# Kernel optimization log

Measured on AMD Instinct MI355X. Metric: run time of the kernel, lower is better.

## Reference

```python
import jax, jax.numpy as jnp
import numpy as np


def setup_inputs() -> dict:
    key = jax.random.key(0)
    ks = jax.random.split(key, 4)
    B, H, W, C = 4, 64, 64, 256
    d = C // 8
    x = jax.random.normal(ks[0], (B, H, W, C), dtype=jnp.float32)
    wq = jax.random.normal(ks[1], (C, d), dtype=jnp.float32) * (1.0 / np.sqrt(C))
    wk = jax.random.normal(ks[2], (C, d), dtype=jnp.float32) * (1.0 / np.sqrt(C))
    wv = jax.random.normal(ks[3], (C, C), dtype=jnp.float32) * (1.0 / np.sqrt(C))
    bq = jnp.zeros((d,), dtype=jnp.float32)
    bk = jnp.zeros((d,), dtype=jnp.float32)
    bv = jnp.zeros((C,), dtype=jnp.float32)
    return {"x": x, "wq": wq, "bq": bq, "wk": wk, "bk": bk, "wv": wv, "bv": bv}


def reference(x, wq, bq, wk, bk, wv, bv):
    # x: [B, H, W, C] (channels-last, as in Keras Conv2D default)
    B, H, W, C = x.shape
    N = H * W
    xf = x.reshape(B, N, C)                      # 1x1 conv == per-pixel matmul
    q = xf @ wq + bq                             # [B, N, C//8]
    k = xf @ wk + bk                             # [B, N, C//8]
    v = xf @ wv + bv                             # [B, N, C]
    # NOTE: original module applies NO 1/sqrt(d) scaling.
    attn = jax.nn.softmax(jnp.einsum('bnd,bmd->bnm', q, k), axis=-1)  # [B, N, N]
    out = jnp.einsum('bnm,bmc->bnc', attn, v)    # [B, N, C]
    return out.reshape(B, H, W, C) + x
```

## Files before the change

kernel.cpp:

```cpp
#include <hip/hip_runtime.h>
#include <stdint.h>

typedef _Float16 f16;
typedef f16 half8 __attribute__((ext_vector_type(8)));
typedef f16 half4 __attribute__((ext_vector_type(4)));
typedef float floatx4 __attribute__((ext_vector_type(4)));

#define MFMA_F16(A, B, Cc) __builtin_amdgcn_mfma_f32_16x16x32_f16((A), (B), (Cc), 0, 0, 0)

static constexpr int NB  = 4;
static constexpr int NN  = 4096;
static constexpr int NC  = 256;
static constexpr int ND  = 32;
static constexpr int PIX = NB * NN;
static constexpr int NS  = 4;
static constexpr int KS  = NN / NS;

__device__ f16 g_WbT[320 * 256];
__device__ f16 g_Qh[(size_t)PIX * ND];
__device__ f16 g_Kh[(size_t)PIX * ND];
__device__ f16 g_VbT[(size_t)NB * NC * NN];
__device__ f16 g_Of[(size_t)NS * PIX * NC];
__device__ float g_m[NS * PIX];
__device__ float g_l[NS * PIX];

__device__ inline void gl2lds16(const f16* g, f16* l) {
  __builtin_amdgcn_global_load_lds(
      (const __attribute__((address_space(1))) void*)g,
      (__attribute__((address_space(3))) void*)l, 16, 0, 0);
}

__global__ __launch_bounds__(256) void prep_weights(const float* __restrict__ wq,
                                                    const float* __restrict__ wk,
                                                    const float* __restrict__ wv) {
  const int tid = blockIdx.x * 256 + threadIdx.x;
  if (tid >= 320 * 256) return;
  const int j = tid >> 8;
  const int k = tid & 255;
  float v;
  if (j < 32)      v = wq[k * 32 + j];
  else if (j < 64) v = wk[k * 32 + (j - 32)];
  else             v = wv[k * 256 + (j - 64)];
  g_WbT[j * 256 + k] = (f16)v;
}

__global__ __launch_bounds__(256) void proj_qkv(const float* __restrict__ x,
                                                const float* __restrict__ bq,
                                                const float* __restrict__ bk,
                                                const float* __restrict__ bv) {
  __shared__ f16 xs[64 * 32];
  __shared__ f16 wsT[160 * 32];
  __shared__ f16 vt[160 * 64];

  const int tid  = threadIdx.x;
  const int lane = tid & 63;
  const int wid  = tid >> 6;
  const int qd   = lane >> 4;
  const int c16  = lane & 15;
  const int p0   = blockIdx.x * 64;
  const int half = blockIdx.y;
  const int j0   = half * 160;
  const floatx4 zero4 = {0.f, 0.f, 0.f, 0.f};

  floatx4 acc[10];
#pragma unroll
  for (int i = 0; i < 10; ++i) acc[i] = zero4;

  for (int kk = 0; kk < 256; kk += 32) {
    {
      const int r = tid >> 2, g = tid & 3;
      const floatx4* s4 = (const floatx4*)(x + (size_t)(p0 + r) * NC + kk + g * 8);
      const floatx4 xa = s4[0], xb = s4[1];
      half8 h;
      h[0] = (f16)xa[0]; h[1] = (f16)xa[1]; h[2] = (f16)xa[2]; h[3] = (f16)xa[3];
      h[4] = (f16)xb[0]; h[5] = (f16)xb[1]; h[6] = (f16)xb[2]; h[7] = (f16)xb[3];
      *(half8*)&xs[r * 32 + g * 8] = h;
    }
#pragma unroll
    for (int i = 0; i < 5; ++i) {
      const int cid = tid + 256 * i;
      const int j = cid >> 3, m = cid & 7;
      *(half4*)&wsT[j * 32 + m * 4] = *(const half4*)&g_WbT[(j0 + j) * 256 + kk + m * 4];
    }
    __syncthreads();
    const half8 a = *(const half8*)&xs[(wid * 16 + c16) * 32 + qd * 8];
#pragma unroll
    for (int nt = 0; nt < 10; ++nt) {
      const half8 bfr = *(const half8*)&wsT[(nt * 16 + c16) * 32 + qd * 8];
      acc[nt] = MFMA_F16(a, bfr, acc[nt]);
    }
    __syncthreads();
  }

#pragma unroll
  for (int nt = 0; nt < 10; ++nt) {
    const int j = j0 + nt * 16 + c16;
    const float bias = (j < 32) ? bq[j] : (j < 64) ? bk[j - 32] : bv[j - 64];
#pragma unroll
    for (int r = 0; r < 4; ++r) {
      const int rl = wid * 16 + qd * 4 + r;
      const int p  = p0 + rl;
      const float val = acc[nt][r] + bias;
      if (j < 32) {
        g_Qh[(size_t)p * ND + j] = (f16)(val * 1.44269504f);
      } else if (j < 64) {
        g_Kh[(size_t)p * ND + (j - 32)] = (f16)val;
      } else {
        vt[(j - 64 - half * 96) * 64 + rl] = (f16)val;
      }
    }
  }
  __syncthreads();
  const int b    = p0 >> 12;
  const int n0   = p0 & (NN - 1);
  const int ncol = half ? 160 : 96;
  const int c0   = half ? 96 : 0;
  const int nit  = (ncol * 16) >> 8;
  for (int i = 0; i < nit; ++i) {
    const int cid = tid + 256 * i;
    const int c = cid >> 4, m = cid & 15;
    *(half4*)(g_VbT + ((size_t)(b * NC + c0 + c)) * NN + n0 + m * 4) =
        *(const half4*)&vt[c * 64 + m * 4];
  }
}

__global__ __launch_bounds__(256, 2) void attn_split(void) {
  __shared__ f16 vsT[256 * 64];
  __shared__ f16 ps[4][2][16 * 64];

  const int tid  = threadIdx.x;
  const int lane = tid & 63;
  const int wid  = tid >> 6;
  const int qd   = lane >> 4;
  const int c16  = lane & 15;
  const int b    = blockIdx.y;
  const int s    = blockIdx.z;
  const int q0   = blockIdx.x * 128 + wid * 32;
  const int sx7  = c16 & 7;
  const floatx4 zero4 = {0.f, 0.f, 0.f, 0.f};

  const int vrow = wid * 64 + (lane >> 3);
  const int vchk = (lane & 7) ^ ((lane >> 3) & 7);
  const f16* vlane = g_VbT + ((size_t)(b * NC + vrow)) * NN + vchk * 8;
  f16* vdst = &vsT[(size_t)wid * 4096 + (size_t)0];

  half8 qf[2];
#pragma unroll
  for (int g = 0; g < 2; ++g)
    qf[g] = *(const half8*)(g_Qh + ((size_t)(b * NN + q0 + g * 16 + c16)) * ND + qd * 8);

  floatx4 acc[2][16];
#pragma unroll
  for (int g = 0; g < 2; ++g)
#pragma unroll
    for (int i = 0; i < 16; ++i) acc[g][i] = zero4;
  float m_i[2] = {-1e30f, -1e30f};
  float l_p[2] = {0.f, 0.f};

  const int kbeg = s * KS, kend = (s + 1) * KS;

#pragma unroll
  for (int i = 0; i < 8; ++i)
    gl2lds16(vlane + kbeg + i * 8 * NN, vdst + i * 512);
  half8 kreg[4];
#pragma unroll
  for (int a = 0; a < 4; ++a)
    kreg[a] = *(const half8*)(g_Kh + ((size_t)(b * NN + kbeg + a * 16 + c16)) * ND + qd * 8);

  for (int k0 = kbeg; k0 < kend; k0 += 64) {
    floatx4 st[2][4];
#pragma unroll
    for (int g = 0; g < 2; ++g)
#pragma unroll
      for (int a = 0; a < 4; ++a) st[g][a] = MFMA_F16(kreg[a], qf[g], zero4);

    float tm[2];
#pragma unroll
    for (int g = 0; g < 2; ++g) {
      float t0 = fmaxf(fmaxf(st[g][0][0], st[g][0][1]), fmaxf(st[g][0][2], st[g][0][3]));
      float t1 = fmaxf(fmaxf(st[g][1][0], st[g][1][1]), fmaxf(st[g][1][2], st[g][1][3]));
      float t2 = fmaxf(fmaxf(st[g][2][0], st[g][2][1]), fmaxf(st[g][2][2], st[g][2][3]));
      float t3 = fmaxf(fmaxf(st[g][3][0], st[g][3][1]), fmaxf(st[g][3][2], st[g][3][3]));
      tm[g] = fmaxf(fmaxf(t0, t1), fmaxf(t2, t3));
    }
    if (__any(tm[0] > m_i[0] || tm[1] > m_i[1])) {
#pragma unroll
      for (int g = 0; g < 2; ++g) {
        float tr = tm[g];
        tr = fmaxf(tr, __shfl_xor(tr, 16));
        tr = fmaxf(tr, __shfl_xor(tr, 32));
        const float m_new = (tr > m_i[g]) ? tr + 5.0f : m_i[g];
        const float alpha = exp2f(m_i[g] - m_new);
        m_i[g] = m_new;
        l_p[g] *= alpha;
        float a4[4];
#pragma unroll
        for (int r = 0; r < 4; ++r) a4[r] = __shfl(alpha, qd * 4 + r);
#pragma unroll
        for (int ct = 0; ct < 16; ++ct)
#pragma unroll
          for (int r = 0; r < 4; ++r) acc[g][ct][r] *= a4[r];
      }
    }

#pragma unroll
    for (int g = 0; g < 2; ++g) {
      float ts = 0.f;
#pragma unroll
      for (int a = 0; a < 4; ++a) {
        half4 h;
#pragma unroll
        for (int r = 0; r < 4; ++r) {
          const float p = exp2f(st[g][a][r] - m_i[g]);
          ts += p;
          h[r] = (f16)p;
        }
        const int pc = ((a * 2 + (qd >> 1)) ^ sx7) * 8 + (qd & 1) * 4;
        *(half4*)&ps[wid][g][c16 * 64 + pc] = h;
      }
      l_p[g] += ts;
    }

    __syncthreads();

    const int k0n = (k0 + 64 < kend) ? (k0 + 64) : kbeg;
    half8 knew[4];
#pragma unroll
    for (int a = 0; a < 4; ++a)
      knew[a] = *(const half8*)(g_Kh + ((size_t)(b * NN + k0n + a * 16 + c16)) * ND + qd * 8);

    half8 pa[2][2];
#pragma unroll
    for (int g = 0; g < 2; ++g)
#pragma unroll
      for (int kh = 0; kh < 2; ++kh)
        pa[g][kh] = *(const half8*)&ps[wid][g][c16 * 64 + ((kh * 4 + qd) ^ sx7) * 8];
#pragma unroll
    for (int ct = 0; ct < 16; ++ct) {
#pragma unroll
      for (int kh = 0; kh < 2; ++kh) {
        const half8 bfr =
            *(const half8*)&vsT[(ct * 16 + c16) * 64 + ((kh * 4 + qd) ^ sx7) * 8];
        acc[0][ct] = MFMA_F16(pa[0][kh], bfr, acc[0][ct]);
        acc[1][ct] = MFMA_F16(pa[1][kh], bfr, acc[1][ct]);
      }
    }
    __syncthreads();

    if (k0 + 64 < kend) {
#pragma unroll
      for (int i = 0; i < 8; ++i)
        gl2lds16(vlane + (k0 + 64) + i * 8 * NN, vdst + i * 512);
    }
#pragma unroll
    for (int a = 0; a < 4; ++a) kreg[a] = knew[a];
  }

#pragma unroll
  for (int g = 0; g < 2; ++g) {
    float l = l_p[g];
    l += __shfl_xor(l, 16);
    l += __shfl_xor(l, 32);
    if (qd == 0) {
      const int row = b * NN + q0 + g * 16 + c16;
      g_m[s * PIX + row] = m_i[g];
      g_l[s * PIX + row] = l;
    }
    float linv[4];
#pragma unroll
    for (int r = 0; r < 4; ++r) linv[r] = 1.0f / __shfl(l, qd * 4 + r);
#pragma unroll
    for (int ct = 0; ct < 16; ++ct)
#pragma unroll
      for (int r = 0; r < 4; ++r) {
        const int qrow = q0 + g * 16 + qd * 4 + r;
        const int c = ct * 16 + c16;
        g_Of[((size_t)(s * PIX + b * NN + qrow)) * NC + c] = (f16)(acc[g][ct][r] * linv[r]);
      }
  }
}

__global__ __launch_bounds__(256) void combine(const float* __restrict__ x,
                                               float* __restrict__ out) {
  const int tid  = threadIdx.x;
  const int lane = tid & 63;
  const int wid  = tid >> 6;
  const int row  = blockIdx.x * 8 + wid * 2 + (lane >> 5);
  const int c    = (lane & 31) * 8;

  float m[NS], l[NS], M = -1e30f;
#pragma unroll
  for (int s = 0; s < NS; ++s) {
    m[s] = g_m[s * PIX + row];
    l[s] = g_l[s * PIX + row];
    M = fmaxf(M, m[s]);
  }
  float w[NS], den = 0.f;
#pragma unroll
  for (int s = 0; s < NS; ++s) { w[s] = l[s] * exp2f(m[s] - M); den += w[s]; }
  const float inv = 1.0f / den;

  float a[8];
#pragma unroll
  for (int j = 0; j < 8; ++j) a[j] = 0.f;
#pragma unroll
  for (int s = 0; s < NS; ++s) {
    const half8 h = *(const half8*)&g_Of[((size_t)(s * PIX + row)) * NC + c];
    const float ws = w[s] * inv;
#pragma unroll
    for (int j = 0; j < 8; ++j) a[j] += ws * (float)h[j];
  }
  const floatx4 x0 = *(const floatx4*)&x[(size_t)row * NC + c];
  const floatx4 x1 = *(const floatx4*)&x[(size_t)row * NC + c + 4];
  floatx4 o0, o1;
#pragma unroll
  for (int j = 0; j < 4; ++j) { o0[j] = a[j] + x0[j]; o1[j] = a[j + 4] + x1[j]; }
  *(floatx4*)&out[(size_t)row * NC + c] = o0;
  *(floatx4*)&out[(size_t)row * NC + c + 4] = o1;
}

extern "C" void kernel_launch(void* const* d_in, const int* in_sizes, int n_in,
                              void* d_out, int out_size, void* d_ws, size_t ws_size,
                              hipStream_t stream) {
  (void)in_sizes; (void)n_in; (void)d_ws; (void)ws_size; (void)out_size;
  const float* x  = (const float*)d_in[0];
  const float* wq = (const float*)d_in[1];
  const float* bq = (const float*)d_in[2];
  const float* wk = (const float*)d_in[3];
  const float* bk = (const float*)d_in[4];
  const float* wv = (const float*)d_in[5];
  const float* bv = (const float*)d_in[6];
  float* out = (float*)d_out;

  hipLaunchKernelGGL(prep_weights, dim3(320), dim3(256), 0, stream, wq, wk, wv);
  hipLaunchKernelGGL(proj_qkv, dim3(256, 2), dim3(256), 0, stream, x, bq, bk, bv);
  hipLaunchKernelGGL(attn_split, dim3(NN / 128, NB, NS), dim3(256), 0, stream);
  hipLaunchKernelGGL(combine, dim3(PIX / 8), dim3(256), 0, stream, x, out);
}
```

Measured before the change: 163.0 us.

## Load projection operands directly from global and vectorize Q/K/V stores via LDS

The projection kernel stops staging x and weight tiles through shared memory. Each lane now loads its MFMA A fragment straight from x and its B fragments straight from the fp16 weight buffer, which removes two barriers per k-step. Q and K outputs are staged in LDS and written with 16-byte row stores instead of scattered 2-byte stores. The V transpose write-out is widened from half4 to half8. Without LDS sharing, each wave re-reads the weights from global/L2, which raises cache traffic.

```diff
diff --git a/kernel.cpp b/kernel.cpp
--- a/kernel.cpp
+++ b/kernel.cpp
@@ -48,9 +48,9 @@
                                                 const float* __restrict__ bq,
                                                 const float* __restrict__ bk,
                                                 const float* __restrict__ bv) {
-  __shared__ f16 xs[64 * 32];
-  __shared__ f16 wsT[160 * 32];
   __shared__ f16 vt[160 * 64];
+  __shared__ f16 qt[64 * 32];
+  __shared__ f16 kt[64 * 32];
 
   const int tid  = threadIdx.x;
   const int lane = tid & 63;
@@ -66,30 +66,21 @@
 #pragma unroll
   for (int i = 0; i < 10; ++i) acc[i] = zero4;
 
+  const float* xrow = x + (size_t)(p0 + wid * 16 + c16) * NC;
+
+#pragma unroll
   for (int kk = 0; kk < 256; kk += 32) {
-    {
-      const int r = tid >> 2, g = tid & 3;
-      const floatx4* s4 = (const floatx4*)(x + (size_t)(p0 + r) * NC + kk + g * 8);
-      const floatx4 xa = s4[0], xb = s4[1];
-      half8 h;
-      h[0] = (f16)xa[0]; h[1] = (f16)xa[1]; h[2] = (f16)xa[2]; h[3] = (f16)xa[3];
-      h[4] = (f16)xb[0]; h[5] = (f16)xb[1]; h[6] = (f16)xb[2]; h[7] = (f16)xb[3];
-      *(half8*)&xs[r * 32 + g * 8] = h;
-    }
-#pragma unroll
-    for (int i = 0; i < 5; ++i) {
-      const int cid = tid + 256 * i;
-      const int j = cid >> 3, m = cid & 7;
-      *(half4*)&wsT[j * 32 + m * 4] = *(const half4*)&g_WbT[(j0 + j) * 256 + kk + m * 4];
-    }
-    __syncthreads();
-    const half8 a = *(const half8*)&xs[(wid * 16 + c16) * 32 + qd * 8];
+    const floatx4* s4 = (const floatx4*)(xrow + kk + qd * 8);
+    const floatx4 xa = s4[0], xb = s4[1];
+    half8 a;
+    a[0] = (f16)xa[0]; a[1] = (f16)xa[1]; a[2] = (f16)xa[2]; a[3] = (f16)xa[3];
+    a[4] = (f16)xb[0]; a[5] = (f16)xb[1]; a[6] = (f16)xb[2]; a[7] = (f16)xb[3];
 #pragma unroll
     for (int nt = 0; nt < 10; ++nt) {
-      const half8 bfr = *(const half8*)&wsT[(nt * 16 + c16) * 32 + qd * 8];
+      const half8 bfr =
+          *(const half8*)&g_WbT[(size_t)(j0 + nt * 16 + c16) * 256 + kk + qd * 8];
       acc[nt] = MFMA_F16(a, bfr, acc[nt]);
     }
-    __syncthreads();
   }
 
 #pragma unroll
@@ -99,28 +90,36 @@
 #pragma unroll
     for (int r = 0; r < 4; ++r) {
       const int rl = wid * 16 + qd * 4 + r;
-      const int p  = p0 + rl;
       const float val = acc[nt][r] + bias;
       if (j < 32) {
-        g_Qh[(size_t)p * ND + j] = (f16)(val * 1.44269504f);
+        qt[rl * 32 + j] = (f16)(val * 1.44269504f);
       } else if (j < 64) {
-        g_Kh[(size_t)p * ND + (j - 32)] = (f16)val;
+        kt[rl * 32 + (j - 32)] = (f16)val;
       } else {
         vt[(j - 64 - half * 96) * 64 + rl] = (f16)val;
       }
     }
   }
   __syncthreads();
+
+  if (half == 0) {
+    const int row = tid >> 2, ch = tid & 3;
+    *(half8*)(g_Qh + (size_t)(p0 + row) * ND + ch * 8) =
+        *(const half8*)&qt[row * 32 + ch * 8];
+    *(half8*)(g_Kh + (size_t)(p0 + row) * ND + ch * 8) =
+        *(const half8*)&kt[row * 32 + ch * 8];
+  }
+
   const int b    = p0 >> 12;
   const int n0   = p0 & (NN - 1);
   const int ncol = half ? 160 : 96;
   const int c0   = half ? 96 : 0;
-  const int nit  = (ncol * 16) >> 8;
+  const int nit  = ncol >> 5;
   for (int i = 0; i < nit; ++i) {
     const int cid = tid + 256 * i;
-    const int c = cid >> 4, m = cid & 15;
-    *(half4*)(g_VbT + ((size_t)(b * NC + c0 + c)) * NN + n0 + m * 4) =
-        *(const half4*)&vt[c * 64 + m * 4];
+    const int c = cid >> 3, m = cid & 7;
+    *(half8*)(g_VbT + ((size_t)(b * NC + c0 + c)) * NN + n0 + m * 8) =
+        *(const half8*)&vt[c * 64 + m * 8];
   }
 }
 
```

Measured after the change: 181.6 us. +11.4%, slower.

## Fuse split-K combine into attention kernel via last-block atomic counter

Applied to the files above, without the earlier changes.

The separate combine kernel is removed. Each attention block now fences its partial results and increments a per-tile atomic counter, and the last of the NS split blocks for a query tile merges the partial outputs with x and writes the final result. This removes one kernel launch and lets the merge overlap with other attention blocks still running. In exchange the merge runs serialized on one block per tile, the block adds fence and atomic overhead, and correctness depends on the counter being reset after each call.

```diff
diff --git a/kernel.cpp b/kernel.cpp
--- a/kernel.cpp
+++ b/kernel.cpp
@@ -23,6 +23,7 @@
 __device__ f16 g_Of[(size_t)NS * PIX * NC];
 __device__ float g_m[NS * PIX];
 __device__ float g_l[NS * PIX];
+__device__ int   g_cnt[NB * (NN / 128)];
 
 __device__ inline void gl2lds16(const f16* g, f16* l) {
   __builtin_amdgcn_global_load_lds(
@@ -124,7 +125,8 @@
   }
 }
 
-__global__ __launch_bounds__(256, 2) void attn_split(void) {
+__global__ __launch_bounds__(256, 2) void attn_split(const float* __restrict__ x,
+                                                     float* __restrict__ out) {
   __shared__ f16 vsT[256 * 64];
   __shared__ f16 ps[4][2][16 * 64];
 
@@ -278,45 +280,65 @@
         g_Of[((size_t)(s * PIX + b * NN + qrow)) * NC + c] = (f16)(acc[g][ct][r] * linv[r]);
       }
   }
-}
-
-__global__ __launch_bounds__(256) void combine(const float* __restrict__ x,
-                                               float* __restrict__ out) {
-  const int tid  = threadIdx.x;
-  const int lane = tid & 63;
-  const int wid  = tid >> 6;
-  const int row  = blockIdx.x * 8 + wid * 2 + (lane >> 5);
-  const int c    = (lane & 31) * 8;
-
-  float m[NS], l[NS], M = -1e30f;
-#pragma unroll
-  for (int s = 0; s < NS; ++s) {
-    m[s] = g_m[s * PIX + row];
-    l[s] = g_l[s * PIX + row];
-    M = fmaxf(M, m[s]);
-  }
-  float w[NS], den = 0.f;
-#pragma unroll
-  for (int s = 0; s < NS; ++s) { w[s] = l[s] * exp2f(m[s] - M); den += w[s]; }
-  const float inv = 1.0f / den;
-
-  float a[8];
-#pragma unroll
-  for (int j = 0; j < 8; ++j) a[j] = 0.f;
-#pragma unroll
-  for (int s = 0; s < NS; ++s) {
-    const half8 h = *(const half8*)&g_Of[((size_t)(s * PIX + row)) * NC + c];
-    const float ws = w[s] * inv;
-#pragma unroll
-    for (int j = 0; j < 8; ++j) a[j] += ws * (float)h[j];
-  }
-  const floatx4 x0 = *(const floatx4*)&x[(size_t)row * NC + c];
-  const floatx4 x1 = *(const floatx4*)&x[(size_t)row * NC + c + 4];
-  floatx4 o0, o1;
-#pragma unroll
-  for (int j = 0; j < 4; ++j) { o0[j] = a[j] + x0[j]; o1[j] = a[j + 4] + x1[j]; }
-  *(floatx4*)&out[(size_t)row * NC + c] = o0;
-  *(floatx4*)&out[(size_t)row * NC + c + 4] = o1;
+
+  __threadfence();
+  __syncthreads();
+  const int cidx = b * (NN / 128) + blockIdx.x;
+  float* wsm   = (float*)&ps[0][0][0];
+  int*   s_old = (int*)(wsm + 512);
+  if (tid == 0) {
+    *s_old = __hip_atomic_fetch_add(&g_cnt[cidx], 1, __ATOMIC_ACQ_REL,
+                                    __HIP_MEMORY_SCOPE_AGENT);
+  }
+  __syncthreads();
+  if (*s_old != NS - 1) return;
+
+  const int rbase = b * NN + blockIdx.x * 128;
+
+  if (tid < 128) {
+    const int row = rbase + tid;
+    float mm[NS], ll[NS], M = -1e30f;
+#pragma unroll
+    for (int sp = 0; sp < NS; ++sp) {
+      mm[sp] = g_m[sp * PIX + row];
+      ll[sp] = g_l[sp * PIX + row];
+      M = fmaxf(M, mm[sp]);
+    }
+    float w[NS], den = 0.f;
+#pragma unroll
+    for (int sp = 0; sp < NS; ++sp) { w[sp] = ll[sp] * exp2f(mm[sp] - M); den += w[sp]; }
+    const float inv = 1.0f / den;
+#pragma unroll
+    for (int sp = 0; sp < NS; ++sp) wsm[tid * 4 + sp] = w[sp] * inv;
+  }
+  __syncthreads();
+
+#pragma unroll
+  for (int i = 0; i < 16; ++i) {
+    const int gi  = tid + 256 * i;
+    const int rl  = gi >> 5;
+    const int cc  = (gi & 31) * 8;
+    const int row = rbase + rl;
+    float a[8];
+#pragma unroll
+    for (int j = 0; j < 8; ++j) a[j] = 0.f;
+#pragma unroll
+    for (int sp = 0; sp < NS; ++sp) {
+      const half8 h = *(const half8*)&g_Of[((size_t)(sp * PIX + row)) * NC + cc];
+      const float ws = wsm[rl * 4 + sp];
+#pragma unroll
+      for (int j = 0; j < 8; ++j) a[j] += ws * (float)h[j];
+    }
+    const floatx4 x0 = *(const floatx4*)&x[(size_t)row * NC + cc];
+    const floatx4 x1 = *(const floatx4*)&x[(size_t)row * NC + cc + 4];
+    floatx4 o0, o1;
+#pragma unroll
+    for (int j = 0; j < 4; ++j) { o0[j] = a[j] + x0[j]; o1[j] = a[j + 4] + x1[j]; }
+    *(floatx4*)&out[(size_t)row * NC + cc] = o0;
+    *(floatx4*)&out[(size_t)row * NC + cc + 4] = o1;
+  }
+
+  if (tid == 0) g_cnt[cidx] = 0;
 }
 
 extern "C" void kernel_launch(void* const* d_in, const int* in_sizes, int n_in,
@@ -334,6 +356,5 @@
 
   hipLaunchKernelGGL(prep_weights, dim3(320), dim3(256), 0, stream, wq, wk, wv);
   hipLaunchKernelGGL(proj_qkv, dim3(256, 2), dim3(256), 0, stream, x, bq, bk, bv);
-  hipLaunchKernelGGL(attn_split, dim3(NN / 128, NB, NS), dim3(256), 0, stream);
-  hipLaunchKernelGGL(combine, dim3(PIX / 8), dim3(256), 0, stream, x, out);
-}
+  hipLaunchKernelGGL(attn_split, dim3(NN / 128, NB, NS), dim3(256), 0, stream, x, out);
+}
```

Result: slower. 275.3 us (+68.9%).

## Double-buffer QKV projection with async LDS loads and split output columns four ways

Applied to the files above, without the earlier changes.

The projection kernel now splits the 320 output columns into four 80-wide slices instead of two 160-wide ones, doubling the grid and lowering per-block accumulator and LDS use so more blocks can be resident. It double-buffers the x and weight tiles: weights are copied straight into LDS with the global-to-LDS helper, and the next x chunk is loaded in registers while MFMAs run on the current chunk. One barrier per step replaces two. The V transpose write-out now uses 8-wide stores. In exchange, each x tile is read and converted twice as often across blocks.

```diff
diff --git a/kernel.cpp b/kernel.cpp
--- a/kernel.cpp
+++ b/kernel.cpp
@@ -44,13 +44,13 @@
   g_WbT[j * 256 + k] = (f16)v;
 }
 
-__global__ __launch_bounds__(256) void proj_qkv(const float* __restrict__ x,
-                                                const float* __restrict__ bq,
-                                                const float* __restrict__ bk,
-                                                const float* __restrict__ bv) {
-  __shared__ f16 xs[64 * 32];
-  __shared__ f16 wsT[160 * 32];
-  __shared__ f16 vt[160 * 64];
+__global__ __launch_bounds__(256, 4) void proj_qkv(const float* __restrict__ x,
+                                                   const float* __restrict__ bq,
+                                                   const float* __restrict__ bk,
+                                                   const float* __restrict__ bv) {
+  __shared__ f16 xs[2][64 * 32];
+  __shared__ f16 wsT[2][80 * 32];
+  __shared__ f16 vt[80 * 64];
 
   const int tid  = threadIdx.x;
   const int lane = tid & 63;
@@ -58,42 +58,62 @@
   const int qd   = lane >> 4;
   const int c16  = lane & 15;
   const int p0   = blockIdx.x * 64;
-  const int half = blockIdx.y;
-  const int j0   = half * 160;
+  const int q    = blockIdx.y;
+  const int j0   = q * 80;
   const floatx4 zero4 = {0.f, 0.f, 0.f, 0.f};
 
-  floatx4 acc[10];
-#pragma unroll
-  for (int i = 0; i < 10; ++i) acc[i] = zero4;
-
-  for (int kk = 0; kk < 256; kk += 32) {
-    {
-      const int r = tid >> 2, g = tid & 3;
-      const floatx4* s4 = (const floatx4*)(x + (size_t)(p0 + r) * NC + kk + g * 8);
-      const floatx4 xa = s4[0], xb = s4[1];
+  const int sr = tid >> 2, sg = tid & 3;
+  const float* xsrc = x + (size_t)(p0 + sr) * NC + sg * 8;
+  const f16* wsrc = g_WbT + (size_t)(j0 + (lane >> 2)) * 256 + (lane & 3) * 8;
+
+  floatx4 acc[5];
+#pragma unroll
+  for (int i = 0; i < 5; ++i) acc[i] = zero4;
+
+  {
+    const floatx4* s4 = (const floatx4*)xsrc;
+    const floatx4 xa = s4[0], xb = s4[1];
+#pragma unroll
+    for (int grp = wid; grp < 5; grp += 4)
+      gl2lds16(wsrc + (size_t)grp * 16 * 256, &wsT[0][grp * 512]);
+    half8 h;
+    h[0] = (f16)xa[0]; h[1] = (f16)xa[1]; h[2] = (f16)xa[2]; h[3] = (f16)xa[3];
+    h[4] = (f16)xb[0]; h[5] = (f16)xb[1]; h[6] = (f16)xb[2]; h[7] = (f16)xb[3];
+    *(half8*)&xs[0][sr * 32 + sg * 8] = h;
+  }
+
+  for (int c = 0; c < 8; ++c) {
+    const int cur = c & 1;
+    __syncthreads();
+
+    floatx4 xa, xb;
+    const bool pf = (c < 7);
+    if (pf) {
+      const floatx4* s4 = (const floatx4*)(xsrc + (c + 1) * 32);
+      xa = s4[0]; xb = s4[1];
+#pragma unroll
+      for (int grp = wid; grp < 5; grp += 4)
+        gl2lds16(wsrc + (size_t)grp * 16 * 256 + (c + 1) * 32,
+                 &wsT[cur ^ 1][grp * 512]);
+    }
+
+    const half8 a = *(const half8*)&xs[cur][(wid * 16 + c16) * 32 + qd * 8];
+#pragma unroll
+    for (int nt = 0; nt < 5; ++nt) {
+      const half8 bfr = *(const half8*)&wsT[cur][(nt * 16 + c16) * 32 + qd * 8];
+      acc[nt] = MFMA_F16(a, bfr, acc[nt]);
+    }
+
+    if (pf) {
       half8 h;
       h[0] = (f16)xa[0]; h[1] = (f16)xa[1]; h[2] = (f16)xa[2]; h[3] = (f16)xa[3];
       h[4] = (f16)xb[0]; h[5] = (f16)xb[1]; h[6] = (f16)xb[2]; h[7] = (f16)xb[3];
-      *(half8*)&xs[r * 32 + g * 8] = h;
-    }
-#pragma unroll
-    for (int i = 0; i < 5; ++i) {
-      const int cid = tid + 256 * i;
-      const int j = cid >> 3, m = cid & 7;
-      *(half4*)&wsT[j * 32 + m * 4] = *(const half4*)&g_WbT[(j0 + j) * 256 + kk + m * 4];
-    }
-    __syncthreads();
-    const half8 a = *(const half8*)&xs[(wid * 16 + c16) * 32 + qd * 8];
-#pragma unroll
-    for (int nt = 0; nt < 10; ++nt) {
-      const half8 bfr = *(const half8*)&wsT[(nt * 16 + c16) * 32 + qd * 8];
-      acc[nt] = MFMA_F16(a, bfr, acc[nt]);
-    }
-    __syncthreads();
-  }
-
-#pragma unroll
-  for (int nt = 0; nt < 10; ++nt) {
+      *(half8*)&xs[cur ^ 1][sr * 32 + sg * 8] = h;
+    }
+  }
+
+#pragma unroll
+  for (int nt = 0; nt < 5; ++nt) {
     const int j = j0 + nt * 16 + c16;
     const float bias = (j < 32) ? bq[j] : (j < 64) ? bk[j - 32] : bv[j - 64];
 #pragma unroll
@@ -106,21 +126,21 @@
       } else if (j < 64) {
         g_Kh[(size_t)p * ND + (j - 32)] = (f16)val;
       } else {
-        vt[(j - 64 - half * 96) * 64 + rl] = (f16)val;
+        const int vloc = (q == 0) ? (nt * 16 + c16 - 64) : (nt * 16 + c16);
+        vt[vloc * 64 + rl] = (f16)val;
       }
     }
   }
   __syncthreads();
+
   const int b    = p0 >> 12;
   const int n0   = p0 & (NN - 1);
-  const int ncol = half ? 160 : 96;
-  const int c0   = half ? 96 : 0;
-  const int nit  = (ncol * 16) >> 8;
-  for (int i = 0; i < nit; ++i) {
-    const int cid = tid + 256 * i;
-    const int c = cid >> 4, m = cid & 15;
-    *(half4*)(g_VbT + ((size_t)(b * NC + c0 + c)) * NN + n0 + m * 4) =
-        *(const half4*)&vt[c * 64 + m * 4];
+  const int vt0  = q ? (80 * q - 64) : 0;
+  const int ncol = q ? 80 : 16;
+  for (int i = tid; i < ncol * 8; i += 256) {
+    const int cc = i >> 3, m = i & 7;
+    *(half8*)(g_VbT + ((size_t)(b * NC + vt0 + cc)) * NN + n0 + m * 8) =
+        *(const half8*)&vt[cc * 64 + m * 8];
   }
 }
 
@@ -333,7 +353,7 @@
   float* out = (float*)d_out;
 
   hipLaunchKernelGGL(prep_weights, dim3(320), dim3(256), 0, stream, wq, wk, wv);
-  hipLaunchKernelGGL(proj_qkv, dim3(256, 2), dim3(256), 0, stream, x, bq, bk, bv);
+  hipLaunchKernelGGL(proj_qkv, dim3(256, 4), dim3(256), 0, stream, x, bq, bk, bv);
   hipLaunchKernelGGL(attn_split, dim3(NN / 128, NB, NS), dim3(256), 0, stream);
   hipLaunchKernelGGL(combine, dim3(PIX / 8), dim3(256), 0, stream, x, out);
 }
```

After: 162.0 us. No clear change (-0.7%).
